# Kernel optimization log

Hardware: AMD Instinct MI355X
Metric: run time of the kernel (lower is better)

## Reference

```python
import jax, jax.numpy as jnp
from jax import lax
import numpy as np

D_STATE = 16
DT_RANK = 16
D_INNER = 512
D_MODEL = 256


def _silu(x):
    return x * jax.nn.sigmoid(x)


def _ln(x, g, b):
    mu = jnp.mean(x, -1, keepdims=True)
    v = jnp.mean((x - mu) ** 2, -1, keepdims=True)
    return (x - mu) / jnp.sqrt(v + 1e-5) * g + b


def _mamba(x, Win, Wc, bc, Wx, Wdt, bdt, Alog, Dp, Wout):
    # x: [B, T, 256]; mamba_ssm defaults: expand=2, d_state=16, d_conv=4
    B, T, _ = x.shape
    xz = x @ Win.T                       # [B,T,1024]
    xc, z = jnp.split(xz, 2, axis=-1)    # each [B,T,512]
    # causal depthwise conv over time
    xt = jnp.transpose(xc, (0, 2, 1))    # [B,512,T]
    xt = lax.conv_general_dilated(xt, Wc[:, None, :], (1,), [(3, 0)],
                                  feature_group_count=D_INNER,
                                  dimension_numbers=('NCH', 'OIH', 'NCH'))
    xc = _silu(jnp.transpose(xt + bc[None, :, None], (0, 2, 1)))  # [B,T,512]
    dbl = xc @ Wx.T                      # [B,T,48]
    dt = jax.nn.softplus(dbl[..., :DT_RANK] @ Wdt.T + bdt)        # [B,T,512]
    Bm = dbl[..., DT_RANK:DT_RANK + D_STATE]                      # [B,T,16]
    Cm = dbl[..., DT_RANK + D_STATE:]                             # [B,T,16]
    A = -jnp.exp(Alog)                   # [512,16]
    dA = jnp.exp(dt[..., None] * A)                               # [B,T,512,16]
    dBu = dt[..., None] * Bm[:, :, None, :] * xc[..., None]       # [B,T,512,16]

    def step(h, inp):
        dA_t, dBu_t, C_t = inp
        h = dA_t * h + dBu_t
        return h, jnp.einsum('bdn,bn->bd', h, C_t)

    h0 = jnp.zeros((B, D_INNER, D_STATE), x.dtype)
    _, ys = lax.scan(step, h0, (jnp.moveaxis(dA, 1, 0),
                                jnp.moveaxis(dBu, 1, 0),
                                jnp.moveaxis(Cm, 1, 0)))
    y = jnp.moveaxis(ys, 0, 1) + xc * Dp
    y = y * _silu(z)
    return y @ Wout.T


def _forward(x1, x2, x3, x4, audio_feature,
             ln_g, ln_b, in_proj_w, conv_w, conv_b, xproj_w,
             dt_w, dt_b, A_log, D, out_proj_w, gate_w, gate_b):
    bt = x1.shape[0]
    gates = []
    for i in range(4):          # 4 independent 3-layer Mamba encoders
        a = audio_feature
        for l in range(3):      # Mamba_channel_temporal_block: a = ln(a); a = a + mamba(a)
            a = _ln(a, ln_g[i, l], ln_b[i, l])
            a = a + _mamba(a, in_proj_w[i, l], conv_w[i, l], conv_b[i, l],
                           xproj_w[i, l], dt_w[i, l], dt_b[i, l],
                           A_log[i, l], D[i, l], out_proj_w[i, l])
        gates.append(_silu(a @ gate_w[i].T + gate_b[i]))  # [B,5,256]
    g1 = gates[0].reshape(bt, 256, 1, 1)
    g2 = jnp.transpose(gates[1], (1, 0, 2)).reshape(bt, 256, 1, 1)
    g3 = jnp.transpose(gates[2], (1, 0, 2)).reshape(bt, 256, 1, 1)
    g4 = jnp.transpose(gates[3], (1, 0, 2)).reshape(bt, 256, 1, 1)
    o1 = x1 + g1 * x1   # gamma = 1
    o2 = x2 + g2 * x2
    o3 = x3 + g3 * x3
    o4 = x4 + g4 * x4
    audio_flat = audio_feature.reshape(-1, D_MODEL)[:, :, None]  # [bt,256,1]
    return (o4, o3, o2, o1, audio_flat)


def setup_inputs() -> dict:
    key = jax.random.key(0)
    ks = jax.random.split(key, 16)
    f32 = jnp.float32
    inp = {
        'x1': jax.random.normal(ks[0], (80, 256, 56, 56), f32),
        'x2': jax.random.normal(ks[1], (80, 256, 28, 28), f32),
        'x3': jax.random.normal(ks[2], (80, 256, 14, 14), f32),
        'x4': jax.random.normal(ks[3], (80, 256, 7, 7), f32),
        'audio_feature': jax.random.normal(ks[4], (16, 5, 256), f32),
        'ln_g': jnp.ones((4, 3, 256), f32),
        'ln_b': jnp.zeros((4, 3, 256), f32),
        'in_proj_w': jax.random.normal(ks[5], (4, 3, 2 * D_INNER, 256), f32) * 0.02,
        'conv_w': jax.random.normal(ks[6], (4, 3, D_INNER, 4), f32) * 0.1,
        'conv_b': jax.random.normal(ks[7], (4, 3, D_INNER), f32) * 0.02,
        'xproj_w': jax.random.normal(ks[8], (4, 3, DT_RANK + 2 * D_STATE, D_INNER), f32) * 0.02,
        'dt_w': jax.random.normal(ks[9], (4, 3, D_INNER, DT_RANK), f32) * 0.02,
        'dt_b': jax.random.normal(ks[10], (4, 3, D_INNER), f32) * 0.1 - 2.0,
        'A_log': jnp.log(jnp.tile(jnp.arange(1, D_STATE + 1, dtype=f32), (4, 3, D_INNER, 1))),
        'D': jnp.ones((4, 3, D_INNER), f32),
        'out_proj_w': jax.random.normal(ks[11], (4, 3, 256, D_INNER), f32) * 0.02,
        'gate_w': jax.random.normal(ks[12], (4, 256, 256), f32) * 0.05,
        'gate_b': jnp.zeros((4, 256), f32),
    }
    return inp


def reference(x1, x2, x3, x4, audio_feature,
              ln_g, ln_b, in_proj_w, conv_w, conv_b, xproj_w,
              dt_w, dt_b, A_log, D, out_proj_w, gate_w, gate_b):
    return _forward(x1, x2, x3, x4, audio_feature,
                    ln_g, ln_b, in_proj_w, conv_w, conv_b, xproj_w,
                    dt_w, dt_b, A_log, D, out_proj_w, gate_w, gate_b)
```

## Files before the change

kernel.cpp:

```cpp
#include <hip/hip_runtime.h>
#include <hip/hip_bf16.h>
#include <math.h>


#define NTOK 80
#define DM   256
#define DI   512

typedef float f32x4 __attribute__((ext_vector_type(4)));

__device__ __forceinline__ float silu_f(float v) {
    return v / (1.f + expf(-v));
}
__device__ __forceinline__ float dot4(float4 a, float4 b) {
    return a.x*b.x + a.y*b.y + a.z*b.z + a.w*b.w;
}

#define OFF_SG    0
#define OFF_WINT  81920
#define OFF_WOUTT 3227648
#define OFF_WXT   4800512
#define OFF_GWT   5095424
#define OFF_DBLP  5357568
#define OFF_OUTP  5419008
#define OFF_BAR   5746688

__global__ __launch_bounds__(256) void k_tr(const float* __restrict__ Win,
                                            const float* __restrict__ Wout,
                                            const float* __restrict__ Wx,
                                            const float* __restrict__ gw,
                                            float* __restrict__ ws) {
    if (blockIdx.x == 0 && threadIdx.x < 256) {
        unsigned* barp = (unsigned*)(ws + OFF_BAR);
        barp[threadIdx.x] = 0u;
        barp[256 + threadIdx.x] = 0u;
    }
    int b = blockIdx.x;
    const float4* src; float4* dst; int R, C4, tile;
    if (b < 768) {
        int mat = b >> 6; tile = b & 63; R = 1024; C4 = 64;
        src = (const float4*)Win + (size_t)mat * 65536;
        dst = (float4*)(ws + OFF_WINT) + (size_t)mat * 65536;
    } else if (b < 1152) {
        int bb = b - 768; int mat = bb >> 5; tile = bb & 31; R = 256; C4 = 128;
        src = (const float4*)Wout + (size_t)mat * 32768;
        dst = (float4*)(ws + OFF_WOUTT) + (size_t)mat * 32768;
    } else if (b < 1248) {
        int bb = b - 1152; int mat = bb >> 3; tile = bb & 7; R = 48; C4 = 128;
        src = (const float4*)Wx + (size_t)mat * 6144;
        dst = (float4*)(ws + OFF_WXT) + (size_t)mat * 6144;
    } else {
        int bb = b - 1248; int mat = bb >> 4; tile = bb & 15; R = 256; C4 = 64;
        src = (const float4*)gw + (size_t)mat * 16384;
        dst = (float4*)(ws + OFF_GWT) + (size_t)mat * 16384;
    }
    int tilesC = C4 >> 5;
    int r0 = (tile / tilesC) << 5, c0 = (tile % tilesC) << 5;
    __shared__ float4 t[32][33];
    int tx = threadIdx.x & 31, ty = threadIdx.x >> 5;
#pragma unroll
    for (int j = 0; j < 4; ++j) {
        int r = ty + j * 8;
        if (r0 + r < R) t[r][tx] = src[(size_t)(r0 + r) * C4 + c0 + tx];
    }
    __syncthreads();
#pragma unroll
    for (int j = 0; j < 4; ++j) {
        int cc = ty + j * 8;
        if (r0 + tx < R) dst[(size_t)(c0 + cc) * R + r0 + tx] = t[tx][cc];
    }
}

__device__ __forceinline__ void gbar(unsigned* slot) {
    __syncthreads();
    if (threadIdx.x == 0) {
        __hip_atomic_fetch_add(slot, 1u, __ATOMIC_RELEASE, __HIP_MEMORY_SCOPE_AGENT);
        while (__hip_atomic_load(slot, __ATOMIC_RELAXED, __HIP_MEMORY_SCOPE_AGENT) < 4u)
            __builtin_amdgcn_s_sleep(1);
        (void)__hip_atomic_load(slot, __ATOMIC_ACQUIRE, __HIP_MEMORY_SCOPE_AGENT);
    }
    __syncthreads();
}

__global__ __launch_bounds__(512) void k_chain4(
    const float* __restrict__ audio,
    const float* __restrict__ ln_g, const float* __restrict__ ln_b,
    const float* __restrict__ Wc,   const float* __restrict__ bc,
    const float* __restrict__ Wdt,  const float* __restrict__ bdt,
    const float* __restrict__ Alog, const float* __restrict__ Dp,
    const float* __restrict__ gb,   float* __restrict__ ws)
{
    int gid = blockIdx.x & 63;
    int q   = blockIdx.x >> 6;
    int i = gid & 3, b = gid >> 2;
    int tid = threadIdx.x, lane = tid & 63, wave = tid >> 6;
    int dq = q * 128;

    float* s_g  = ws + OFF_SG;
    float* dblp = ws + OFF_DBLP + (size_t)gid * 4 * 240;
    float* outp = ws + OFF_OUTP + (size_t)gid * 4 * 1280;
    unsigned* bar = (unsigned*)(ws + OFF_BAR) + gid * 8;

    __shared__ __align__(16) float a_l   [1280];
    __shared__ __align__(16) float aln_l [1280];
    __shared__ __align__(16) float xz_l  [1280];
    __shared__ __align__(16) float xc_l  [640];
    __shared__ __align__(16) float y_l   [640];
    __shared__ __align__(16) float dbl_l [240];
    __shared__ __align__(16) float part_l[2560];

    for (int v = tid; v < 320; v += 512)
        ((float4*)a_l)[v] = ((const float4*)(audio + (size_t)b * 1280))[v];
    __syncthreads();

    for (int l = 0; l < 3; ++l) {
        int il = i * 3 + l;

        if (wave < 5) {
            float4 x = ((float4*)a_l)[wave*64 + lane];
            float s = x.x + x.y + x.z + x.w;
            #pragma unroll
            for (int o = 32; o > 0; o >>= 1) s += __shfl_down(s, o, 64);
            float mu = __shfl(s, 0, 64) * (1.f/256.f);
            float4 d = make_float4(x.x-mu, x.y-mu, x.z-mu, x.w-mu);
            float v2 = d.x*d.x + d.y*d.y + d.z*d.z + d.w*d.w;
            #pragma unroll
            for (int o = 32; o > 0; o >>= 1) v2 += __shfl_down(v2, o, 64);
            float rstd = rsqrtf(__shfl(v2, 0, 64) * (1.f/256.f) + 1e-5f);
            float4 g4 = ((const float4*)(ln_g + (size_t)il*DM))[lane];
            float4 b4 = ((const float4*)(ln_b + (size_t)il*DM))[lane];
            ((float4*)aln_l)[wave*64 + lane] =
                make_float4(d.x*rstd*g4.x + b4.x, d.y*rstd*g4.y + b4.y,
                            d.z*rstd*g4.z + b4.z, d.w*rstd*g4.w + b4.w);
        }
        __syncthreads();

        {
            int cl = tid & 255, kh = tid >> 8;
            int gcol = (cl < 128) ? (dq + cl) : (384 + dq + cl);
            const float4* wp = (const float4*)(ws + OFF_WINT) + (size_t)il*65536 + gcol;
            const float4* a4 = (const float4*)aln_l;
            float ac0=0.f, ac1=0.f, ac2=0.f, ac3=0.f, ac4=0.f;
            #pragma unroll 8
            for (int kk = 0; kk < 32; ++kk) {
                int k4 = kh*32 + kk;
                float4 w = wp[(size_t)k4*1024];
                ac0 += dot4(w, a4[k4]);      ac1 += dot4(w, a4[64+k4]);
                ac2 += dot4(w, a4[128+k4]);  ac3 += dot4(w, a4[192+k4]);
                ac4 += dot4(w, a4[256+k4]);
            }
            part_l[kh*1280 +       cl] = ac0;  part_l[kh*1280 + 256 + cl] = ac1;
            part_l[kh*1280 + 512 + cl] = ac2;  part_l[kh*1280 + 768 + cl] = ac3;
            part_l[kh*1280 +1024 + cl] = ac4;
        }
        __syncthreads();
        for (int v = tid; v < 1280; v += 512) xz_l[v] = part_l[v] + part_l[1280 + v];
        __syncthreads();

        for (int v = tid; v < 640; v += 512) {
            int r = v >> 7, dl = v & 127;
            int d = dq + dl;
            float acc = bc[(size_t)il*DI + d];
            const float* wr = Wc + ((size_t)il*DI + d)*4;
            #pragma unroll
            for (int k = 0; k < 4; ++k) {
                int ts = r + k - 3;
                if (ts >= 0) acc += wr[k] * xz_l[ts*256 + dl];
            }
            xc_l[r*128 + dl] = silu_f(acc);
        }
        __syncthreads();

        if (tid < 480) {
            int c = tid % 48, r = (tid / 48) % 5, kh = tid / 240;
            const float4* wp = (const float4*)(ws + OFF_WXT) + (size_t)il*6144 + c;
            const float4* x4 = (const float4*)xc_l + r*32 + kh*16;
            float acc = 0.f;
            #pragma unroll 8
            for (int kk = 0; kk < 16; ++kk)
                acc += dot4(wp[(size_t)(q*32 + kh*16 + kk)*48], x4[kk]);
            part_l[tid] = acc;
        }
        __syncthreads();
        if (tid < 240) dblp[q*240 + tid] = part_l[tid] + part_l[240 + tid];
        gbar(bar + l*2);
        if (tid < 240)
            dbl_l[tid] = dblp[tid] + dblp[240+tid] + dblp[480+tid] + dblp[720+tid];
        __syncthreads();

        if (tid < 128) {
            int d = dq + tid;
            float A[16], h[16];
            const float4* al4 = (const float4*)(Alog + ((size_t)il*DI + d)*16);
            float4 av0 = al4[0], av1 = al4[1], av2 = al4[2], av3 = al4[3];
            A[0]=-expf(av0.x); A[1]=-expf(av0.y); A[2]=-expf(av0.z); A[3]=-expf(av0.w);
            A[4]=-expf(av1.x); A[5]=-expf(av1.y); A[6]=-expf(av1.z); A[7]=-expf(av1.w);
            A[8]=-expf(av2.x); A[9]=-expf(av2.y); A[10]=-expf(av2.z); A[11]=-expf(av2.w);
            A[12]=-expf(av3.x); A[13]=-expf(av3.y); A[14]=-expf(av3.z); A[15]=-expf(av3.w);
            #pragma unroll
            for (int n = 0; n < 16; ++n) h[n] = 0.f;
            const float4* wd4 = (const float4*)(Wdt + ((size_t)il*DI + d)*16);
            float4 w0 = wd4[0], w1 = wd4[1], w2 = wd4[2], w3 = wd4[3];
            float bdtv = bdt[(size_t)il*DI + d];
            float dv   = Dp[(size_t)il*DI + d];
            #pragma unroll
            for (int t = 0; t < 5; ++t) {
                const float* db = dbl_l + t*48;
                float acc = bdtv;
                acc += db[0]*w0.x + db[1]*w0.y + db[2]*w0.z + db[3]*w0.w;
                acc += db[4]*w1.x + db[5]*w1.y + db[6]*w1.z + db[7]*w1.w;
                acc += db[8]*w2.x + db[9]*w2.y + db[10]*w2.z + db[11]*w2.w;
                acc += db[12]*w3.x + db[13]*w3.y + db[14]*w3.z + db[15]*w3.w;
                float dtv = fmaxf(acc, 0.f) + log1pf(expf(-fabsf(acc)));
                float xv  = xc_l[t*128 + tid];
                float zv  = xz_l[t*256 + 128 + tid];
                float dx  = dtv * xv;
                float yacc = 0.f;
                #pragma unroll
                for (int n = 0; n < 16; ++n) {
                    h[n] = expf(dtv*A[n])*h[n] + dx*db[16 + n];
                    yacc += h[n]*db[32 + n];
                }
                y_l[t*128 + tid] = (yacc + xv*dv) * silu_f(zv);
            }
        }
        __syncthreads();

        {
            int c = tid & 255, kh = tid >> 8;
            const float4* wp = (const float4*)(ws + OFF_WOUTT) + (size_t)il*32768 + c;
            const float4* yy = (const float4*)y_l;
            float ac0=0.f, ac1=0.f, ac2=0.f, ac3=0.f, ac4=0.f;
            #pragma unroll 8
            for (int kk = 0; kk < 16; ++kk) {
                int k4 = q*32 + kh*16 + kk;
                int yk = kh*16 + kk;
                float4 w = wp[(size_t)k4*256];
                ac0 += dot4(w, yy[yk]);      ac1 += dot4(w, yy[32+yk]);
                ac2 += dot4(w, yy[64+yk]);   ac3 += dot4(w, yy[96+yk]);
                ac4 += dot4(w, yy[128+yk]);
            }
            part_l[kh*1280 +       c] = ac0;  part_l[kh*1280 + 256 + c] = ac1;
            part_l[kh*1280 + 512 + c] = ac2;  part_l[kh*1280 + 768 + c] = ac3;
            part_l[kh*1280 +1024 + c] = ac4;
        }
        __syncthreads();
        for (int v = tid; v < 1280; v += 512)
            outp[q*1280 + v] = part_l[v] + part_l[1280 + v];
        gbar(bar + l*2 + 1);
        for (int v = tid; v < 1280; v += 512)
            a_l[v] = aln_l[v] + outp[v] + outp[1280+v] + outp[2560+v] + outp[3840+v];
        __syncthreads();
    }

    {
        int cl = tid & 63, kq = tid >> 6;
        int cg = q*64 + cl;
        const float4* wp = (const float4*)(ws + OFF_GWT) + (size_t)i*16384 + cg;
        const float4* a4 = (const float4*)a_l;
        float ac0=0.f, ac1=0.f, ac2=0.f, ac3=0.f, ac4=0.f;
        #pragma unroll 8
        for (int kk = 0; kk < 8; ++kk) {
            int k4 = kq*8 + kk;
            float4 w = wp[(size_t)k4*256];
            ac0 += dot4(w, a4[k4]);      ac1 += dot4(w, a4[64+k4]);
            ac2 += dot4(w, a4[128+k4]);  ac3 += dot4(w, a4[192+k4]);
            ac4 += dot4(w, a4[256+k4]);
        }
        part_l[kq*320 +       cl] = ac0;  part_l[kq*320 +  64 + cl] = ac1;
        part_l[kq*320 + 128 + cl] = ac2;  part_l[kq*320 + 192 + cl] = ac3;
        part_l[kq*320 + 256 + cl] = ac4;
    }
    __syncthreads();
    for (int v = tid; v < 320; v += 512) {
        int r = v >> 6, cl = v & 63;
        int cg = q*64 + cl;
        float acc = gb[(size_t)i*DM + cg];
        #pragma unroll
        for (int kq = 0; kq < 8; ++kq) acc += part_l[kq*320 + v];
        int row = b*5 + r;
        int np  = (i == 0) ? row : (r*16 + b);
        s_g[((size_t)i*NTOK + np)*DM + cg] = 1.f + silu_f(acc);
    }
}

__global__ __launch_bounds__(256) void k_elem(
    const float* __restrict__ x1, const float* __restrict__ x2,
    const float* __restrict__ x3, const float* __restrict__ x4,
    const float* __restrict__ audio, const float* __restrict__ s_g,
    float* __restrict__ out) {
    int b = blockIdx.x;
    int t = threadIdx.x;

    if (b < 512) {
        const float* s = s_g + 3 * NTOK * DM;
        const f32x4* xv = (const f32x4*)x4;
        f32x4* ov = (f32x4*)out;
        const int total4 = 1003520 / 4;
        for (int v = b * 256 + t; v < total4; v += 512 * 256) {
            f32x4 x = __builtin_nontemporal_load(&xv[v]);
#pragma unroll
            for (int j = 0; j < 4; ++j) {
                int idx = v * 4 + j;
                x[j] *= s[idx / 49];
            }
            __builtin_nontemporal_store(x, &ov[v]);
        }
    } else if (b < 1024) {
        const float* s = s_g + 2 * NTOK * DM;
        const f32x4* xv = (const f32x4*)x3;
        f32x4* ov = (f32x4*)(out + 1003520);
        const int total4 = 4014080 / 4;
        for (int v = (b - 512) * 256 + t; v < total4; v += 512 * 256) {
            float f = s[v / 49];
            f32x4 x = __builtin_nontemporal_load(&xv[v]);
            x *= f;
            __builtin_nontemporal_store(x, &ov[v]);
        }
    } else if (b < 2048) {
        const float* s = s_g + 1 * NTOK * DM;
        const f32x4* xv = (const f32x4*)x2;
        f32x4* ov = (f32x4*)(out + 5017600);
        const int total4 = 16056320 / 4;
        for (int v = (b - 1024) * 256 + t; v < total4; v += 1024 * 256) {
            float f = s[v / 196];
            f32x4 x = __builtin_nontemporal_load(&xv[v]);
            x *= f;
            __builtin_nontemporal_store(x, &ov[v]);
        }
    } else if (b < 6144) {
        const float* s = s_g;
        const f32x4* xv = (const f32x4*)x1;
        f32x4* ov = (f32x4*)(out + 21073920);
        const int total4 = 64225280 / 4;
        for (int v = (b - 2048) * 256 + t; v < total4; v += 4096 * 256) {
            float f = s[v / 784];
            f32x4 x = __builtin_nontemporal_load(&xv[v]);
            x *= f;
            __builtin_nontemporal_store(x, &ov[v]);
        }
    } else {
        int idx = (b - 6144) * 256 + t;
        out[85299200 + idx] = audio[idx];
    }
}

extern "C" void kernel_launch(void* const* d_in, const int* in_sizes, int n_in,
                              void* d_out, int out_size, void* d_ws, size_t ws_size,
                              hipStream_t stream) {
    const float* x1        = (const float*)d_in[0];
    const float* x2        = (const float*)d_in[1];
    const float* x3        = (const float*)d_in[2];
    const float* x4        = (const float*)d_in[3];
    const float* audio     = (const float*)d_in[4];
    const float* ln_g      = (const float*)d_in[5];
    const float* ln_b      = (const float*)d_in[6];
    const float* in_proj_w = (const float*)d_in[7];
    const float* conv_w    = (const float*)d_in[8];
    const float* conv_b    = (const float*)d_in[9];
    const float* xproj_w   = (const float*)d_in[10];
    const float* dt_w      = (const float*)d_in[11];
    const float* dt_b      = (const float*)d_in[12];
    const float* A_log     = (const float*)d_in[13];
    const float* Dvec      = (const float*)d_in[14];
    const float* out_proj_w= (const float*)d_in[15];
    const float* gate_w    = (const float*)d_in[16];
    const float* gate_b    = (const float*)d_in[17];

    float* ws = (float*)d_ws;

    k_tr<<<1312, 256, 0, stream>>>(in_proj_w, out_proj_w, xproj_w, gate_w, ws);
    k_chain4<<<256, 512, 0, stream>>>(audio, ln_g, ln_b, conv_w, conv_b,
                                      dt_w, dt_b, A_log, Dvec, gate_b, ws);
    k_elem<<<6224, 256, 0, stream>>>(x1, x2, x3, x4, audio, ws + OFF_SG,
                                     (float*)d_out);
}
```

Measured before the change: 252.4 us.

## Exchange conv output across quarter-blocks once per layer to halve grid barriers

Each of the four blocks cooperating on one (encoder, batch) pair now publishes its conv-activated xc and z slices to global scratch and passes one barrier. After that every block holds the full 512-channel xc/z, so it computes the whole x_proj, scan and out_proj redundantly. This removes the second cross-block barrier and the partial-sum exchanges for dbl and out_proj. In return each block does four times the x_proj/scan/out_proj work and reads the full Wout slice, with larger shared-memory buffers.

Result: slower. 308.5 us (+22.2%).

```diff
diff --git a/kernel.cpp b/kernel.cpp
--- a/kernel.cpp
+++ b/kernel.cpp
@@ -21,19 +21,18 @@
 #define OFF_WOUTT 3227648
 #define OFF_WXT   4800512
 #define OFF_GWT   5095424
-#define OFF_DBLP  5357568
-#define OFF_OUTP  5419008
-#define OFF_BAR   5746688
+#define OFF_XCZP  5357568
+#define OFF_BAR   5685248
 
 __global__ __launch_bounds__(256) void k_tr(const float* __restrict__ Win,
                                             const float* __restrict__ Wout,
                                             const float* __restrict__ Wx,
                                             const float* __restrict__ gw,
                                             float* __restrict__ ws) {
-    if (blockIdx.x == 0 && threadIdx.x < 256) {
+    if (blockIdx.x == 0) {
         unsigned* barp = (unsigned*)(ws + OFF_BAR);
-        barp[threadIdx.x] = 0u;
-        barp[256 + threadIdx.x] = 0u;
+        #pragma unroll
+        for (int j = 0; j < 4; ++j) barp[j * 256 + threadIdx.x] = 0u;
     }
     int b = blockIdx.x;
     const float4* src; float4* dst; int R, C4, tile;
@@ -97,15 +96,15 @@
     int dq = q * 128;
 
     float* s_g  = ws + OFF_SG;
-    float* dblp = ws + OFF_DBLP + (size_t)gid * 4 * 240;
-    float* outp = ws + OFF_OUTP + (size_t)gid * 4 * 1280;
-    unsigned* bar = (unsigned*)(ws + OFF_BAR) + gid * 8;
+    float* xczp = ws + OFF_XCZP + (size_t)gid * 5120;
+    unsigned* bar = (unsigned*)(ws + OFF_BAR) + gid * 16;
 
     __shared__ __align__(16) float a_l   [1280];
     __shared__ __align__(16) float aln_l [1280];
     __shared__ __align__(16) float xz_l  [1280];
-    __shared__ __align__(16) float xc_l  [640];
-    __shared__ __align__(16) float y_l   [640];
+    __shared__ __align__(16) float xc_f  [2560];
+    __shared__ __align__(16) float z_f   [2560];
+    __shared__ __align__(16) float y_f   [2560];
     __shared__ __align__(16) float dbl_l [240];
     __shared__ __align__(16) float part_l[2560];
 
@@ -157,39 +156,52 @@
         for (int v = tid; v < 1280; v += 512) xz_l[v] = part_l[v] + part_l[1280 + v];
         __syncthreads();
 
-        for (int v = tid; v < 640; v += 512) {
-            int r = v >> 7, dl = v & 127;
-            int d = dq + dl;
-            float acc = bc[(size_t)il*DI + d];
-            const float* wr = Wc + ((size_t)il*DI + d)*4;
-            #pragma unroll
-            for (int k = 0; k < 4; ++k) {
-                int ts = r + k - 3;
-                if (ts >= 0) acc += wr[k] * xz_l[ts*256 + dl];
-            }
-            xc_l[r*128 + dl] = silu_f(acc);
-        }
+        for (int v = tid; v < 1280; v += 512) {
+            int r = v >> 8, c = v & 255;
+            float val;
+            if (c < 128) {
+                int d = dq + c;
+                float acc = bc[(size_t)il*DI + d];
+                const float* wr = Wc + ((size_t)il*DI + d)*4;
+                #pragma unroll
+                for (int k = 0; k < 4; ++k) {
+                    int ts = r + k - 3;
+                    if (ts >= 0) acc += wr[k] * xz_l[ts*256 + c];
+                }
+                val = silu_f(acc);
+            } else {
+                val = xz_l[v];
+            }
+            xczp[q*1280 + v] = val;
+        }
+        gbar(bar + l);
+
+        #pragma unroll
+        for (int q2 = 0; q2 < 4; ++q2)
+            for (int v = tid; v < 1280; v += 512) {
+                int r = v >> 8, c = v & 255;
+                float val = xczp[q2*1280 + v];
+                if (c < 128) xc_f[r*512 + q2*128 + c] = val;
+                else         z_f [r*512 + q2*128 + (c & 127)] = val;
+            }
         __syncthreads();
 
         if (tid < 480) {
             int c = tid % 48, r = (tid / 48) % 5, kh = tid / 240;
             const float4* wp = (const float4*)(ws + OFF_WXT) + (size_t)il*6144 + c;
-            const float4* x4 = (const float4*)xc_l + r*32 + kh*16;
+            const float4* x4 = (const float4*)xc_f + r*128 + kh*64;
             float acc = 0.f;
             #pragma unroll 8
-            for (int kk = 0; kk < 16; ++kk)
-                acc += dot4(wp[(size_t)(q*32 + kh*16 + kk)*48], x4[kk]);
+            for (int kk = 0; kk < 64; ++kk)
+                acc += dot4(wp[(size_t)(kh*64 + kk)*48], x4[kk]);
             part_l[tid] = acc;
         }
         __syncthreads();
-        if (tid < 240) dblp[q*240 + tid] = part_l[tid] + part_l[240 + tid];
-        gbar(bar + l*2);
-        if (tid < 240)
-            dbl_l[tid] = dblp[tid] + dblp[240+tid] + dblp[480+tid] + dblp[720+tid];
-        __syncthreads();
-
-        if (tid < 128) {
-            int d = dq + tid;
+        if (tid < 240) dbl_l[tid] = part_l[tid] + part_l[240 + tid];
+        __syncthreads();
+
+        {
+            int d = tid;
             float A[16], h[16];
             const float4* al4 = (const float4*)(Alog + ((size_t)il*DI + d)*16);
             float4 av0 = al4[0], av1 = al4[1], av2 = al4[2], av3 = al4[3];
@@ -212,8 +224,8 @@
                 acc += db[8]*w2.x + db[9]*w2.y + db[10]*w2.z + db[11]*w2.w;
                 acc += db[12]*w3.x + db[13]*w3.y + db[14]*w3.z + db[15]*w3.w;
                 float dtv = fmaxf(acc, 0.f) + log1pf(expf(-fabsf(acc)));
-                float xv  = xc_l[t*128 + tid];
-                float zv  = xz_l[t*256 + 128 + tid];
+                float xv  = xc_f[t*512 + d];
+                float zv  = z_f [t*512 + d];
                 float dx  = dtv * xv;
                 float yacc = 0.f;
                 #pragma unroll
@@ -221,7 +233,7 @@
                     h[n] = expf(dtv*A[n])*h[n] + dx*db[16 + n];
                     yacc += h[n]*db[32 + n];
                 }
-                y_l[t*128 + tid] = (yacc + xv*dv) * silu_f(zv);
+                y_f[t*512 + d] = (yacc + xv*dv) * silu_f(zv);
             }
         }
         __syncthreads();
@@ -229,16 +241,15 @@
         {
             int c = tid & 255, kh = tid >> 8;
             const float4* wp = (const float4*)(ws + OFF_WOUTT) + (size_t)il*32768 + c;
-            const float4* yy = (const float4*)y_l;
+            const float4* yy = (const float4*)y_f;
             float ac0=0.f, ac1=0.f, ac2=0.f, ac3=0.f, ac4=0.f;
             #pragma unroll 8
-            for (int kk = 0; kk < 16; ++kk) {
-                int k4 = q*32 + kh*16 + kk;
-                int yk = kh*16 + kk;
+            for (int kk = 0; kk < 64; ++kk) {
+                int k4 = kh*64 + kk;
                 float4 w = wp[(size_t)k4*256];
-                ac0 += dot4(w, yy[yk]);      ac1 += dot4(w, yy[32+yk]);
-                ac2 += dot4(w, yy[64+yk]);   ac3 += dot4(w, yy[96+yk]);
-                ac4 += dot4(w, yy[128+yk]);
+                ac0 += dot4(w, yy[k4]);      ac1 += dot4(w, yy[128+k4]);
+                ac2 += dot4(w, yy[256+k4]);  ac3 += dot4(w, yy[384+k4]);
+                ac4 += dot4(w, yy[512+k4]);
             }
             part_l[kh*1280 +       c] = ac0;  part_l[kh*1280 + 256 + c] = ac1;
             part_l[kh*1280 + 512 + c] = ac2;  part_l[kh*1280 + 768 + c] = ac3;
@@ -246,10 +257,7 @@
         }
         __syncthreads();
         for (int v = tid; v < 1280; v += 512)
-            outp[q*1280 + v] = part_l[v] + part_l[1280 + v];
-        gbar(bar + l*2 + 1);
-        for (int v = tid; v < 1280; v += 512)
-            a_l[v] = aln_l[v] + outp[v] + outp[1280+v] + outp[2560+v] + outp[3840+v];
+            a_l[v] = aln_l[v] + part_l[v] + part_l[1280 + v];
         __syncthreads();
     }
 
```
